# Performance work log

Measured on AMD Instinct MI355X. Metric: run time of the kernel, lower is better.

## Reference

```python
import jax, jax.numpy as jnp
import numpy as np

# fp4 e2m1 positive value grid and midpoints between adjacent grid values
_GRID = jnp.array([0.0, 0.5, 1.0, 1.5, 2.0, 3.0, 4.0, 6.0], dtype=jnp.float32)
_MIDS = jnp.array([0.25, 0.75, 1.25, 1.75, 2.5, 3.5, 5.0], dtype=jnp.float32)
BLOCK = 32               # MX block size
E8M0_BIAS = 127
F32_MIN_NORMAL = float(2.0 ** -126)
F4_E2M1_MAX_POW2 = 2     # log2 of largest power-of-two <= 6.0 -> 4.0


def _quantize_fp4(a):
    """Round-to-nearest-even onto the signed e2m1 grid."""
    mag = jnp.clip(jnp.abs(a), 0.0, 6.0)
    idx = jnp.searchsorted(_MIDS, mag, side='left')  # ties round down
    mids_pad = jnp.concatenate([_MIDS, jnp.array([-1.0], jnp.float32)])
    tie = mag == mids_pad[idx]
    idx = jnp.where(tie & (idx % 2 == 1), idx + 1, idx)  # ties-to-even mantissa
    return _GRID[idx] * jnp.where(a < 0, -1.0, 1.0)


def _floor_log2(m):
    """Exact floor(log2(m)) for m > 0, with corrections for fp rounding of log2."""
    e = jnp.floor(jnp.log2(m))
    e = jnp.where(jnp.exp2(e) > m, e - 1.0, e)
    e = jnp.where(jnp.exp2(e + 1.0) <= m, e + 1.0, e)
    return e


def _qdq_mxfp4(x):
    """Quantize-dequantize x to MX fp4_e2m1, block 32, FLOOR scale mode (to_mx + to_dtype)."""
    shp = x.shape
    xb = x.reshape(-1, BLOCK)
    max_abs = jnp.max(jnp.abs(xb), axis=1)
    eps = F32_MIN_NORMAL * (max_abs == 0).astype(jnp.float32)
    pow2 = _floor_log2(max_abs + eps)
    e_unb = jnp.clip(pow2 - F4_E2M1_MAX_POW2, -float(E8M0_BIAS), float(E8M0_BIAS) + 1.0)
    scale = jnp.maximum(jnp.exp2(e_unb), F32_MIN_NORMAL)  # [nblk]
    q = _quantize_fp4(xb / scale[:, None])
    return (q * scale[:, None]).reshape(shp)


def _dequant_weight(weight_packed, weight_scale, out_f, in_f):
    """Unpack uint8-packed fp4 (low nibble first), apply e8m0 block scales."""
    p = weight_packed.astype(jnp.int32)
    low = p & 0xF
    high = (p >> 4) & 0xF
    nib = jnp.stack([low, high], axis=-1).reshape(out_f, in_f)  # interleave low,high
    vals = _GRID[nib & 7] * jnp.where((nib & 8) > 0, -1.0, 1.0)
    s = jnp.exp2(weight_scale.astype(jnp.float32) - E8M0_BIAS)  # get_fp_scale(e8m0)
    return (vals.reshape(-1, BLOCK) * s[:, None]).reshape(out_f, in_f)


def setup_inputs() -> dict:
    key = jax.random.key(0)
    k1, k2, k3 = jax.random.split(key, 3)
    M, IN, OUT = 4096, 4096, 4096
    x = jax.random.normal(k1, (M, IN), dtype=jnp.float32)
    weight_packed = jax.random.randint(k2, (OUT, IN // 2), 0, 256, dtype=jnp.int32)
    weight_scale = jax.random.randint(k3, (OUT * IN // BLOCK,), 0, 135, dtype=jnp.int32)
    return {"x": x, "weight_packed": weight_packed, "weight_scale": weight_scale}


def reference(x, weight_packed, weight_scale):
    out_f = weight_packed.shape[0]
    in_f = weight_packed.shape[1] * 2
    xq = _qdq_mxfp4(x)                                       # qdq_mxfp4(x)
    w_dq = _dequant_weight(weight_packed, weight_scale, out_f, in_f)
    return xq @ w_dq.T                                       # matmul(x, w_dq.t())
```

## Files before the change

### kernel.cpp

```cpp
#include <hip/hip_runtime.h>
#include <stdint.h>

typedef __attribute__((ext_vector_type(4)))  int   intx4;
typedef __attribute__((ext_vector_type(8)))  int   intx8;
typedef __attribute__((ext_vector_type(16))) float floatx16;

#define GLL16(gp, lp)                                                               \
    __builtin_amdgcn_global_load_lds((const __attribute__((address_space(1))) unsigned int*)(gp), \
                                     (__attribute__((address_space(3))) unsigned int*)(lp), 16, 0, 0)
#define GLL4(gp, lp)                                                                \
    __builtin_amdgcn_global_load_lds((const __attribute__((address_space(1))) unsigned int*)(gp), \
                                     (__attribute__((address_space(3))) unsigned int*)(lp), 4, 0, 0)

__device__ __forceinline__ uint32_t enc1(float xv, float inv) {
    float a = fminf(fabsf(xv) * inv, 6.0f);
    int e;
    if (a < 2.0f)      e = (int)rintf(a + a);
    else if (a < 4.0f) e = (int)rintf(a) + 2;
    else               e = (int)rintf(a * 0.5f) + 4;
    return (uint32_t)e | ((__float_as_uint(xv) >> 28) & 8u);
}

__global__ __launch_bounds__(256) void quant_x_kernel(const float* __restrict__ x,
                                                      uint32_t* __restrict__ xq,
                                                      uint8_t* __restrict__ xs) {
    const int gl = blockIdx.x * 256 + threadIdx.x;
    const float4 v = ((const float4*)x)[gl];
    float m = fmaxf(fmaxf(fabsf(v.x), fabsf(v.y)), fmaxf(fabsf(v.z), fabsf(v.w)));
    m = fmaxf(m, __shfl_xor(m, 1));
    m = fmaxf(m, __shfl_xor(m, 2));
    m = fmaxf(m, __shfl_xor(m, 4));
    const unsigned ef = __float_as_uint(m) >> 23;
    const unsigned code = (ef < 3u) ? 1u : (ef - 2u);
    const float inv = __uint_as_float((254u - code) << 23);
    const uint32_t p = enc1(v.x, inv)        | (enc1(v.y, inv) << 4)
                     | (enc1(v.z, inv) << 8) | (enc1(v.w, inv) << 12);
    ((uint16_t*)xq)[gl] = (uint16_t)p;
    if ((gl & 7) == 0) xs[gl >> 3] = (uint8_t)code;
}

__global__ __launch_bounds__(256) void repack_kernel(const int* __restrict__ wp,
                                                     uint32_t* __restrict__ wrep,
                                                     int n4w,
                                                     const int* __restrict__ wsc,
                                                     uint32_t* __restrict__ ws,
                                                     int n4s) {
    const int t = blockIdx.x * 256 + threadIdx.x;
    if (t < n4w) {
        const int4 p = ((const int4*)wp)[t];
        wrep[t] = (uint32_t)(p.x & 0xFF) | ((uint32_t)(p.y & 0xFF) << 8)
                | ((uint32_t)(p.z & 0xFF) << 16) | ((uint32_t)(p.w & 0xFF) << 24);
    } else if (t - n4w < n4s) {
        const int i = t - n4w;
        const int4 p = ((const int4*)wsc)[i];
        ws[i] = (uint32_t)(p.x & 0xFF) | ((uint32_t)(p.y & 0xFF) << 8)
              | ((uint32_t)(p.z & 0xFF) << 16) | ((uint32_t)(p.w & 0xFF) << 24);
    }
}

__global__ __launch_bounds__(256) void gemm_mx_kernel(const uint8_t* __restrict__ Apk,
                                                      const uint8_t* __restrict__ Bpk,
                                                      const uint8_t* __restrict__ As,
                                                      const uint8_t* __restrict__ Bs,
                                                      float* __restrict__ C,
                                                      int M, int N, int K) {
    __shared__ __align__(16) uint8_t sA[2][8192];
    __shared__ __align__(16) uint8_t sB[2][8192];
    __shared__ __align__(16) uint8_t sS[2][1024];

    const int tid = threadIdx.x;
    const int bm0 = blockIdx.y << 7;
    const int bn0 = blockIdx.x << 7;
    const int wave = tid >> 6;
    const int lane = tid & 63;
    const int wm = (wave >> 1) << 6;
    const int wn = (wave & 1) << 6;
    const int row = lane & 31;
    const int h = lane >> 5;
    const int Kb = K >> 1;
    const int kbpr = K >> 5;

    const int s0 = tid, s1 = tid + 256;
    const int r0 = s0 >> 2, p0 = (s0 & 3) ^ (r0 & 3);
    const int r1 = s1 >> 2, p1 = (s1 & 3) ^ (r1 & 3);
    const uint8_t* Ag0 = Apk + (size_t)(bm0 + r0) * Kb + p0 * 16;
    const uint8_t* Ag1 = Apk + (size_t)(bm0 + r1) * Kb + p1 * 16;
    const uint8_t* Bg0 = Bpk + (size_t)(bn0 + r0) * Kb + p0 * 16;
    const uint8_t* Bg1 = Bpk + (size_t)(bn0 + r1) * Kb + p1 * 16;

    const int srow = tid & 127;
    const uint8_t* Sg = (tid < 128) ? (As + (size_t)(bm0 + srow) * kbpr)
                                    : (Bs + (size_t)(bn0 + srow) * kbpr);
    const int sldoff = ((tid < 128) ? 0 : 512) + srow * 4;

    floatx16 acc[2][2];
#pragma unroll
    for (int a = 0; a < 2; ++a)
#pragma unroll
        for (int b = 0; b < 2; ++b)
#pragma unroll
            for (int r = 0; r < 16; ++r) acc[a][b][r] = 0.f;

    const int nchunk = K >> 7;

    auto STAGE = [&](int bf, int c) {
        const size_t koff = (size_t)c << 6;
        GLL16(Ag0 + koff, &sA[bf][s0 * 16]);
        GLL16(Ag1 + koff, &sA[bf][s1 * 16]);
        GLL16(Bg0 + koff, &sB[bf][s0 * 16]);
        GLL16(Bg1 + koff, &sB[bf][s1 * 16]);
        GLL4(Sg + (size_t)c * 4, &sS[bf][sldoff]);
    };

    const int ar0 = wm + row, ar1 = wm + 32 + row;
    const int br0 = wn + row, br1 = wn + 32 + row;

    auto COMPUTE = [&](int bf) {
        const uint32_t saw0 = *(const uint32_t*)&sS[bf][ar0 * 4];
        const uint32_t saw1 = *(const uint32_t*)&sS[bf][ar1 * 4];
        const uint32_t sbw0 = *(const uint32_t*)&sS[bf][512 + br0 * 4];
        const uint32_t sbw1 = *(const uint32_t*)&sS[bf][512 + br1 * 4];
#pragma unroll
        for (int s = 0; s < 2; ++s) {
            const int kp = 2 * s + h;
            const int sh = kp * 8;
            intx4 a4[2], b4[2];
            a4[0] = *(const intx4*)&sA[bf][ar0 * 64 + ((kp ^ (ar0 & 3)) << 4)];
            a4[1] = *(const intx4*)&sA[bf][ar1 * 64 + ((kp ^ (ar1 & 3)) << 4)];
            b4[0] = *(const intx4*)&sB[bf][br0 * 64 + ((kp ^ (br0 & 3)) << 4)];
            b4[1] = *(const intx4*)&sB[bf][br1 * 64 + ((kp ^ (br1 & 3)) << 4)];
            const int sa[2] = { (int)((saw0 >> sh) & 0xFF), (int)((saw1 >> sh) & 0xFF) };
            const int sb[2] = { (int)((sbw0 >> sh) & 0xFF), (int)((sbw1 >> sh) & 0xFF) };
            __builtin_amdgcn_s_setprio(1);
#pragma unroll
            for (int mt = 0; mt < 2; ++mt)
#pragma unroll
                for (int nt = 0; nt < 2; ++nt) {
                    intx8 a8 = {a4[mt][0], a4[mt][1], a4[mt][2], a4[mt][3], 0, 0, 0, 0};
                    intx8 b8 = {b4[nt][0], b4[nt][1], b4[nt][2], b4[nt][3], 0, 0, 0, 0};
                    acc[mt][nt] = __builtin_amdgcn_mfma_scale_f32_32x32x64_f8f6f4(
                        a8, b8, acc[mt][nt], 4, 4, 0, sa[mt], 0, sb[nt]);
                }
            __builtin_amdgcn_s_setprio(0);
        }
    };

    STAGE(0, 0);
    for (int c = 0; c < nchunk - 1; ++c) {
        const int bf = c & 1;
        STAGE(bf ^ 1, c + 1);
        asm volatile("s_waitcnt vmcnt(5)" ::: "memory");
        __builtin_amdgcn_s_barrier();
        COMPUTE(bf);
        __builtin_amdgcn_s_barrier();
    }
    asm volatile("s_waitcnt vmcnt(0)" ::: "memory");
    __builtin_amdgcn_s_barrier();
    COMPUTE((nchunk - 1) & 1);

#pragma unroll
    for (int mt = 0; mt < 2; ++mt)
#pragma unroll
        for (int nt = 0; nt < 2; ++nt) {
            const int col = bn0 + wn + nt * 32 + row;
#pragma unroll
            for (int g = 0; g < 4; ++g) {
                const int rw = bm0 + wm + mt * 32 + 8 * g + 4 * h;
#pragma unroll
                for (int q = 0; q < 4; ++q)
                    C[(size_t)(rw + q) * N + col] = acc[mt][nt][4 * g + q];
            }
        }
}

extern "C" void kernel_launch(void* const* d_in, const int* in_sizes, int n_in,
                              void* d_out, int out_size, void* d_ws, size_t ws_size,
                              hipStream_t stream) {
    const float* x = (const float*)d_in[0];
    const int* wp = (const int*)d_in[1];
    const int* wsc = (const int*)d_in[2];
    float* out = (float*)d_out;

    const int K = 4096;
    const int M = in_sizes[0] / K;
    const int N = (in_sizes[1] * 2) / K;
    const int kbpr = K / 32;
    const int npack = N * K / 2;

    uint32_t* xq   = (uint32_t*)d_ws;
    uint8_t*  xs   = (uint8_t*)d_ws + (size_t)M * K / 2;
    uint8_t*  ws   = xs + (size_t)M * kbpr;
    uint32_t* wrep = (uint32_t*)(ws + (size_t)N * kbpr);

    const int n4w = npack / 4;
    const int n4s = (N * kbpr) / 4;

    quant_x_kernel<<<(M * K / 4) / 256, 256, 0, stream>>>(x, xq, xs);
    repack_kernel<<<(n4w + n4s + 255) / 256, 256, 0, stream>>>(wp, wrep, n4w,
                                                               wsc, (uint32_t*)ws, n4s);

    dim3 grid(N / 128, M / 128);
    gemm_mx_kernel<<<grid, 256, 0, stream>>>((const uint8_t*)xq, (const uint8_t*)wrep,
                                             xs, ws, out, M, N, K);
}
```

Before: 210.7 us.

## Replace double-buffered LDS pipeline with single-buffer sync loop and new swizzle

Removes the double-buffered prefetch pipeline in the MX fp4 GEMM and uses a single LDS buffer with __syncthreads around each chunk's global-to-LDS load. It also changes the LDS XOR swizzle to use (row>>1)&3, loads per-k scale bytes directly instead of extracting them from packed words, and drops s_setprio. This halves LDS usage, which may allow more resident blocks, but it loses the overlap of memory loads with MFMA compute.

```diff
diff --git a/kernel.cpp b/kernel.cpp
--- a/kernel.cpp
+++ b/kernel.cpp
@@ -64,9 +64,9 @@
                                                       const uint8_t* __restrict__ Bs,
                                                       float* __restrict__ C,
                                                       int M, int N, int K) {
-    __shared__ __align__(16) uint8_t sA[2][8192];
-    __shared__ __align__(16) uint8_t sB[2][8192];
-    __shared__ __align__(16) uint8_t sS[2][1024];
+    __shared__ __align__(16) uint8_t sA[8192];
+    __shared__ __align__(16) uint8_t sB[8192];
+    __shared__ __align__(16) uint8_t sS[1024];
 
     const int tid = threadIdx.x;
     const int bm0 = blockIdx.y << 7;
@@ -81,8 +81,8 @@
     const int kbpr = K >> 5;
 
     const int s0 = tid, s1 = tid + 256;
-    const int r0 = s0 >> 2, p0 = (s0 & 3) ^ (r0 & 3);
-    const int r1 = s1 >> 2, p1 = (s1 & 3) ^ (r1 & 3);
+    const int r0 = s0 >> 2, p0 = (s0 & 3) ^ ((r0 >> 1) & 3);
+    const int r1 = s1 >> 2, p1 = (s1 & 3) ^ ((r1 >> 1) & 3);
     const uint8_t* Ag0 = Apk + (size_t)(bm0 + r0) * Kb + p0 * 16;
     const uint8_t* Ag1 = Apk + (size_t)(bm0 + r1) * Kb + p1 * 16;
     const uint8_t* Bg0 = Bpk + (size_t)(bn0 + r0) * Kb + p0 * 16;
@@ -102,36 +102,32 @@
             for (int r = 0; r < 16; ++r) acc[a][b][r] = 0.f;
 
     const int nchunk = K >> 7;
-
-    auto STAGE = [&](int bf, int c) {
-        const size_t koff = (size_t)c << 6;
-        GLL16(Ag0 + koff, &sA[bf][s0 * 16]);
-        GLL16(Ag1 + koff, &sA[bf][s1 * 16]);
-        GLL16(Bg0 + koff, &sB[bf][s0 * 16]);
-        GLL16(Bg1 + koff, &sB[bf][s1 * 16]);
-        GLL4(Sg + (size_t)c * 4, &sS[bf][sldoff]);
-    };
-
     const int ar0 = wm + row, ar1 = wm + 32 + row;
     const int br0 = wn + row, br1 = wn + 32 + row;
 
-    auto COMPUTE = [&](int bf) {
-        const uint32_t saw0 = *(const uint32_t*)&sS[bf][ar0 * 4];
-        const uint32_t saw1 = *(const uint32_t*)&sS[bf][ar1 * 4];
-        const uint32_t sbw0 = *(const uint32_t*)&sS[bf][512 + br0 * 4];
-        const uint32_t sbw1 = *(const uint32_t*)&sS[bf][512 + br1 * 4];
+    for (int c = 0; c < nchunk; ++c) {
+        __syncthreads();
+        const size_t koff = (size_t)c << 6;
+        GLL16(Ag0 + koff, sA + s0 * 16);
+        GLL16(Ag1 + koff, sA + s1 * 16);
+        GLL16(Bg0 + koff, sB + s0 * 16);
+        GLL16(Bg1 + koff, sB + s1 * 16);
+        GLL4(Sg + (size_t)c * 4, sS + sldoff);
+        __syncthreads();
+
 #pragma unroll
         for (int s = 0; s < 2; ++s) {
             const int kp = 2 * s + h;
-            const int sh = kp * 8;
             intx4 a4[2], b4[2];
-            a4[0] = *(const intx4*)&sA[bf][ar0 * 64 + ((kp ^ (ar0 & 3)) << 4)];
-            a4[1] = *(const intx4*)&sA[bf][ar1 * 64 + ((kp ^ (ar1 & 3)) << 4)];
-            b4[0] = *(const intx4*)&sB[bf][br0 * 64 + ((kp ^ (br0 & 3)) << 4)];
-            b4[1] = *(const intx4*)&sB[bf][br1 * 64 + ((kp ^ (br1 & 3)) << 4)];
-            const int sa[2] = { (int)((saw0 >> sh) & 0xFF), (int)((saw1 >> sh) & 0xFF) };
-            const int sb[2] = { (int)((sbw0 >> sh) & 0xFF), (int)((sbw1 >> sh) & 0xFF) };
-            __builtin_amdgcn_s_setprio(1);
+            int sa[2], sb[2];
+            a4[0] = *(const intx4*)(sA + ar0 * 64 + ((kp ^ ((ar0 >> 1) & 3)) << 4));
+            a4[1] = *(const intx4*)(sA + ar1 * 64 + ((kp ^ ((ar1 >> 1) & 3)) << 4));
+            b4[0] = *(const intx4*)(sB + br0 * 64 + ((kp ^ ((br0 >> 1) & 3)) << 4));
+            b4[1] = *(const intx4*)(sB + br1 * 64 + ((kp ^ ((br1 >> 1) & 3)) << 4));
+            sa[0] = sS[ar0 * 4 + kp];
+            sa[1] = sS[ar1 * 4 + kp];
+            sb[0] = sS[512 + br0 * 4 + kp];
+            sb[1] = sS[512 + br1 * 4 + kp];
 #pragma unroll
             for (int mt = 0; mt < 2; ++mt)
 #pragma unroll
@@ -141,22 +137,8 @@
                     acc[mt][nt] = __builtin_amdgcn_mfma_scale_f32_32x32x64_f8f6f4(
                         a8, b8, acc[mt][nt], 4, 4, 0, sa[mt], 0, sb[nt]);
                 }
-            __builtin_amdgcn_s_setprio(0);
         }
-    };
-
-    STAGE(0, 0);
-    for (int c = 0; c < nchunk - 1; ++c) {
-        const int bf = c & 1;
-        STAGE(bf ^ 1, c + 1);
-        asm volatile("s_waitcnt vmcnt(5)" ::: "memory");
-        __builtin_amdgcn_s_barrier();
-        COMPUTE(bf);
-        __builtin_amdgcn_s_barrier();
     }
-    asm volatile("s_waitcnt vmcnt(0)" ::: "memory");
-    __builtin_amdgcn_s_barrier();
-    COMPUTE((nchunk - 1) & 1);
 
 #pragma unroll
     for (int mt = 0; mt < 2; ++mt)
```

Result: no change. 212.6 us (+0.9%).
